# Optimization experiments

Hardware: AMD Instinct MI355X
Metric: run time of the kernel (lower is better)

The kernel has to match this reference:

```python
import jax, jax.numpy as jnp
import numpy as np

N_SAMPLES = 8_000_000
N_TRAIN = 1_000_000
KS = 9
HALF_KS = (KS - 1) // 2  # 4
SIGMA = 1.0


def _build_stats():
    """Replicates LDSLoss.__init__: histogramdd, gaussian LDS smoothing, scaling."""
    rng = np.random.default_rng(0)
    labels = rng.uniform(0.0, 10.0, size=(N_TRAIN, 2))
    n_bins = int((labels.max() - labels.min()) / 0.1)
    hist, edges = np.histogramdd(labels, bins=n_bins)
    # gaussian_filter1d(impulse, sigma)/max == exp(-0.5*(x/sigma)^2), truncated at 4*sigma (= half_ks)
    x = np.arange(-HALF_KS, HALF_KS + 1, dtype=np.float64)
    kernel = np.exp(-0.5 * (x / SIGMA) ** 2)
    # scipy.ndimage.convolve1d(hist, kernel, mode='constant') acts along the LAST axis only;
    # kernel is symmetric so convolution == correlation.
    pad = np.pad(hist, ((0, 0), (HALF_KS, HALF_KS)))
    smoothed = np.zeros_like(hist)
    for k in range(KS):
        smoothed += kernel[k] * pad[:, k:k + n_bins]
    bins0 = edges[0]
    bins1 = edges[1]
    # scaling = len(w)/sum(w) with w = 1/smoothed[bin(label)] over the training labels
    i0 = np.clip(np.searchsorted(bins0, labels[:, 0], side='right') - 1, 0, n_bins - 1)
    i1 = np.clip(np.searchsorted(bins1, labels[:, 1], side='right') - 1, 0, n_bins - 1)
    w = 1.0 / smoothed[i0, i1]
    scaling = len(w) / w.sum()
    lo = np.array([bins0[0], bins1[0]])
    hi = np.array([bins0[-1], bins1[-1]])
    return (smoothed.astype(np.float32), bins0.astype(np.float32),
            bins1.astype(np.float32), np.float32(scaling), lo, hi)


def setup_inputs() -> dict:
    smoothed, bins0, bins1, scaling, lo, hi = _build_stats()
    key = jax.random.key(0)
    k1, k2 = jax.random.split(key)
    inp = jax.random.normal(k1, (N_SAMPLES, 2), dtype=jnp.float32)
    # targets drawn inside the training-label range (as histogram bins cover it)
    tgt = jax.random.uniform(k2, (N_SAMPLES, 2), dtype=jnp.float32,
                             minval=jnp.asarray(lo, jnp.float32),
                             maxval=jnp.asarray(hi, jnp.float32))
    return {
        "input": inp,
        "target": tgt,
        "smoothed_distribution": jnp.asarray(smoothed),
        "bins0": jnp.asarray(bins0),
        "bins1": jnp.asarray(bins1),
        "scaling": jnp.asarray(scaling),
    }


def reference(input, target, smoothed_distribution, bins0, bins1, scaling):
    nb = smoothed_distribution.shape[0]
    # torch.where(label < bins)[0][0] - 1  ==  searchsorted(bins, label, 'right') - 1,
    # with the 'no edge greater' case mapped to the last bin (len(bins)-2).
    i0 = jnp.clip(jnp.searchsorted(bins0, target[:, 0], side='right') - 1, 0, nb - 1)
    i1 = jnp.clip(jnp.searchsorted(bins1, target[:, 1], side='right') - 1, 0, nb - 1)
    kernel_weights = smoothed_distribution[i0, i1]          # irregular gather  [N]
    weights = 1.0 / kernel_weights
    inf_mask = jnp.isinf(weights)
    finite_max = jnp.max(jnp.where(inf_mask, -jnp.inf, weights))
    weights = jnp.where(inf_mask, finite_max, weights) * scaling
    loss = (input - target) ** 2                             # MSELoss(reduction='none')
    loss = loss * weights[:, None]
    return jnp.mean(loss)
```

## Files before the change

### kernel.cpp

```cpp
#include <hip/hip_runtime.h>
#include <math.h>


#define BLOCK 1024
#define GRID_BLKS 512

__device__ __forceinline__ int find_bin(const float* __restrict__ sb, int nb,
                                        float x, float lo, float inv_step) {
    int g = (int)floorf((x - lo) * inv_step);
    g = g < 0 ? 0 : (g > nb - 1 ? nb - 1 : g);
    float e0 = sb[g];
    float e1 = sb[g + 1];
    g += (x >= e1) ? 1 : 0;
    g -= (x < e0) ? 1 : 0;
    return g < 0 ? 0 : (g > nb - 1 ? nb - 1 : g);
}

__device__ __forceinline__ void process_pair(
    float4 in, float4 tg,
    float* __restrict__ hist,
    const float* __restrict__ sb0, const float* __restrict__ sb1, int nb,
    float lo0, float inv0, float lo1, float inv1)
{
    float dA0 = in.x - tg.x, dA1 = in.y - tg.y;
    float sqA = dA0 * dA0 + dA1 * dA1;
    int iA0 = find_bin(sb0, nb, tg.x, lo0, inv0);
    int iA1 = find_bin(sb1, nb, tg.y, lo1, inv1);
    atomicAdd(&hist[iA0 * nb + iA1], sqA);

    float dB0 = in.z - tg.z, dB1 = in.w - tg.w;
    float sqB = dB0 * dB0 + dB1 * dB1;
    int iB0 = find_bin(sb0, nb, tg.z, lo0, inv0);
    int iB1 = find_bin(sb1, nb, tg.w, lo1, inv1);
    atomicAdd(&hist[iB0 * nb + iB1], sqB);
}

__global__ void __launch_bounds__(BLOCK, 8)
lds_loss_hist(const float* __restrict__ input,
              const float* __restrict__ target,
              const float* __restrict__ smoothed,
              const float* __restrict__ bins0,
              const float* __restrict__ bins1,
              const float* __restrict__ scaling,
              int nb, long long n, long long nelem,
              double* __restrict__ accA,
              double* __restrict__ accB,
              unsigned int* __restrict__ accM,
              unsigned int* __restrict__ done_ctr,
              float* __restrict__ out)
{
    extern __shared__ __align__(16) float smem[];
    float* hist = smem;
    float* sb0  = smem + nb * nb;
    float* sb1  = sb0 + (nb + 1);

    const int nbnb = nb * nb;
    for (int i = threadIdx.x; i < nbnb; i += BLOCK) hist[i] = 0.0f;
    for (int i = threadIdx.x; i < nb + 1; i += BLOCK) {
        sb0[i] = bins0[i];
        sb1[i] = bins1[i];
    }
    __syncthreads();

    const float lo0 = sb0[0], inv0 = (float)nb / (sb0[nb] - sb0[0]);
    const float lo1 = sb1[0], inv1 = (float)nb / (sb1[nb] - sb1[0]);

    const long long npair = n >> 1;
    const float4* in4 = (const float4*)input;
    const float4* tg4 = (const float4*)target;
    const long long S = (long long)gridDim.x * BLOCK;
    const long long STEP = 2 * S;

    long long base = (long long)blockIdx.x * BLOCK + threadIdx.x;

    float4 ai0, ai1, at0, at1;
    float4 bi0, bi1, bt0, bt1;

    bool haveA = (base + S) < npair;
    if (haveA) {
        ai0 = in4[base]; ai1 = in4[base + S];
        at0 = tg4[base]; at1 = tg4[base + S];
    }
    while (haveA) {
        long long nxtB = base + STEP;
        bool haveB = (nxtB + S) < npair;
        if (haveB) {
            bi0 = in4[nxtB]; bi1 = in4[nxtB + S];
            bt0 = tg4[nxtB]; bt1 = tg4[nxtB + S];
        }
        __builtin_amdgcn_sched_barrier(0);
        process_pair(ai0, at0, hist, sb0, sb1, nb, lo0, inv0, lo1, inv1);
        process_pair(ai1, at1, hist, sb0, sb1, nb, lo0, inv0, lo1, inv1);
        if (!haveB) { base = nxtB; haveA = false; break; }

        long long nxtA = nxtB + STEP;
        haveA = (nxtA + S) < npair;
        if (haveA) {
            ai0 = in4[nxtA]; ai1 = in4[nxtA + S];
            at0 = tg4[nxtA]; at1 = tg4[nxtA + S];
        }
        __builtin_amdgcn_sched_barrier(0);
        process_pair(bi0, bt0, hist, sb0, sb1, nb, lo0, inv0, lo1, inv1);
        process_pair(bi1, bt1, hist, sb0, sb1, nb, lo0, inv0, lo1, inv1);
        base = nxtA;
    }
    for (long long r = base; r < npair; r += S) {
        process_pair(in4[r], tg4[r], hist, sb0, sb1, nb, lo0, inv0, lo1, inv1);
    }

    if ((n & 1) && blockIdx.x == 0 && threadIdx.x == 0) {
        long long i = n - 1;
        float t0 = target[2 * i], t1 = target[2 * i + 1];
        float d0 = input[2 * i] - t0, d1 = input[2 * i + 1] - t1;
        float sq = d0 * d0 + d1 * d1;
        int j0 = find_bin(sb0, nb, t0, lo0, inv0);
        int j1 = find_bin(sb1, nb, t1, lo1, inv1);
        atomicAdd(&hist[j0 * nb + j1], sq);
    }
    __syncthreads();

    double A = 0.0, B = 0.0;
    float  m = 0.0f;
    for (int b = threadIdx.x; b < nbnb; b += BLOCK) {
        float h = hist[b];
        float s = smoothed[b];
        float w = 1.0f / s;
        if (isinf(w)) {
            B += (double)h;
        } else {
            A += (double)w * (double)h;
            if (h > 0.0f) m = fmaxf(m, w);
        }
    }

    #pragma unroll
    for (int off = 32; off > 0; off >>= 1) {
        A += __shfl_down(A, off, 64);
        B += __shfl_down(B, off, 64);
        m = fmaxf(m, __shfl_down(m, off, 64));
    }

    __shared__ double rA[BLOCK / 64], rB[BLOCK / 64];
    __shared__ float  rM[BLOCK / 64];
    int wave = threadIdx.x >> 6;
    int lane = threadIdx.x & 63;
    if (lane == 0) { rA[wave] = A; rB[wave] = B; rM[wave] = m; }
    __syncthreads();

    if (threadIdx.x == 0) {
        double ta = 0.0, tb = 0.0; float tm = 0.0f;
        #pragma unroll
        for (int w2 = 0; w2 < BLOCK / 64; ++w2) {
            ta += rA[w2]; tb += rB[w2]; tm = fmaxf(tm, rM[w2]);
        }
        atomicAdd(accA, ta);
        atomicAdd(accB, tb);
        atomicMax(accM, __float_as_uint(tm));
        __threadfence();
        unsigned int prev = atomicAdd(done_ctr, 1u);
        if (prev == gridDim.x - 1) {
            double Af = atomicAdd(accA, 0.0);
            double Bf = atomicAdd(accB, 0.0);
            float  Mf = __uint_as_float(atomicMax(accM, 0u));
            double v = (double)(*scaling) * (Af + (double)Mf * Bf) / (double)nelem;
            *out = (float)v;
        }
    }
}

extern "C" void kernel_launch(void* const* d_in, const int* in_sizes, int n_in,
                              void* d_out, int out_size, void* d_ws, size_t ws_size,
                              hipStream_t stream) {
    const float* input    = (const float*)d_in[0];
    const float* target   = (const float*)d_in[1];
    const float* smoothed = (const float*)d_in[2];
    const float* bins0    = (const float*)d_in[3];
    const float* bins1    = (const float*)d_in[4];
    const float* scaling  = (const float*)d_in[5];

    const long long nelem = in_sizes[0];
    const long long n     = nelem / 2;
    const int nb          = in_sizes[3] - 1;

    double*       accA = (double*)d_ws;
    double*       accB = accA + 1;
    unsigned int* accM = (unsigned int*)(accB + 1);
    unsigned int* ctr  = accM + 1;

    hipMemsetAsync(d_ws, 0, 24, stream);

    long long blocks_needed = (n / 2 + BLOCK - 1) / BLOCK;
    int grid = (int)(blocks_needed < GRID_BLKS ? blocks_needed : GRID_BLKS);
    if (grid < 1) grid = 1;
    size_t shmem = ((size_t)nb * nb + 2 * (nb + 1)) * sizeof(float);

    lds_loss_hist<<<grid, BLOCK, shmem, stream>>>(
        input, target, smoothed, bins0, bins1, scaling,
        nb, n, nelem, accA, accB, accM, ctr, (float*)d_out);
}
```

Measured before the change: 188.7 us.

## Pack bin edges as float2, halve block size, use 4-way unrolled load loop

Stores bin edge pairs as float2 in LDS so each bin lookup does one 8-byte LDS read instead of two scalar reads. Replaces the double-buffered A/B prefetch loop with a simpler loop that issues four float4 loads per stream before processing. Changes block size to 512 with grid 1024, giving more blocks and more per-block LDS histograms (each histogram is about 40KB, so LDS limits blocks per CU). The cost is more per-block histogram init and final reduction work, and less cross-iteration prefetch overlap.

```diff
diff --git a/kernel.cpp b/kernel.cpp
--- a/kernel.cpp
+++ b/kernel.cpp
@@ -2,40 +2,39 @@
 #include <math.h>
 
 
-#define BLOCK 1024
-#define GRID_BLKS 512
+#define BLOCK 512
+#define GRID_BLKS 1024
 
-__device__ __forceinline__ int find_bin(const float* __restrict__ sb, int nb,
+__device__ __forceinline__ int find_bin(const float2* __restrict__ ep, int nb,
                                         float x, float lo, float inv_step) {
     int g = (int)floorf((x - lo) * inv_step);
     g = g < 0 ? 0 : (g > nb - 1 ? nb - 1 : g);
-    float e0 = sb[g];
-    float e1 = sb[g + 1];
-    g += (x >= e1) ? 1 : 0;
-    g -= (x < e0) ? 1 : 0;
+    float2 e = ep[g];
+    g += (x >= e.y) ? 1 : 0;
+    g -= (x < e.x) ? 1 : 0;
     return g < 0 ? 0 : (g > nb - 1 ? nb - 1 : g);
 }
 
 __device__ __forceinline__ void process_pair(
     float4 in, float4 tg,
     float* __restrict__ hist,
-    const float* __restrict__ sb0, const float* __restrict__ sb1, int nb,
+    const float2* __restrict__ ep0, const float2* __restrict__ ep1, int nb,
     float lo0, float inv0, float lo1, float inv1)
 {
     float dA0 = in.x - tg.x, dA1 = in.y - tg.y;
     float sqA = dA0 * dA0 + dA1 * dA1;
-    int iA0 = find_bin(sb0, nb, tg.x, lo0, inv0);
-    int iA1 = find_bin(sb1, nb, tg.y, lo1, inv1);
+    int iA0 = find_bin(ep0, nb, tg.x, lo0, inv0);
+    int iA1 = find_bin(ep1, nb, tg.y, lo1, inv1);
     atomicAdd(&hist[iA0 * nb + iA1], sqA);
 
     float dB0 = in.z - tg.z, dB1 = in.w - tg.w;
     float sqB = dB0 * dB0 + dB1 * dB1;
-    int iB0 = find_bin(sb0, nb, tg.z, lo0, inv0);
-    int iB1 = find_bin(sb1, nb, tg.w, lo1, inv1);
+    int iB0 = find_bin(ep0, nb, tg.z, lo0, inv0);
+    int iB1 = find_bin(ep1, nb, tg.w, lo1, inv1);
     atomicAdd(&hist[iB0 * nb + iB1], sqB);
 }
 
-__global__ void __launch_bounds__(BLOCK, 8)
+__global__ void __launch_bounds__(BLOCK, 4)
 lds_loss_hist(const float* __restrict__ input,
               const float* __restrict__ target,
               const float* __restrict__ smoothed,
@@ -50,62 +49,47 @@
               float* __restrict__ out)
 {
     extern __shared__ __align__(16) float smem[];
-    float* hist = smem;
-    float* sb0  = smem + nb * nb;
-    float* sb1  = sb0 + (nb + 1);
+    float2* ep0  = (float2*)smem;
+    float2* ep1  = ep0 + nb;
+    float*  hist = (float*)(ep1 + nb);
 
     const int nbnb = nb * nb;
     for (int i = threadIdx.x; i < nbnb; i += BLOCK) hist[i] = 0.0f;
-    for (int i = threadIdx.x; i < nb + 1; i += BLOCK) {
-        sb0[i] = bins0[i];
-        sb1[i] = bins1[i];
+    for (int i = threadIdx.x; i < nb; i += BLOCK) {
+        ep0[i] = make_float2(bins0[i], bins0[i + 1]);
+        ep1[i] = make_float2(bins1[i], bins1[i + 1]);
     }
     __syncthreads();
 
-    const float lo0 = sb0[0], inv0 = (float)nb / (sb0[nb] - sb0[0]);
-    const float lo1 = sb1[0], inv1 = (float)nb / (sb1[nb] - sb1[0]);
+    const float lo0 = ep0[0].x, hi0 = ep0[nb - 1].y;
+    const float lo1 = ep1[0].x, hi1 = ep1[nb - 1].y;
+    const float inv0 = (float)nb / (hi0 - lo0);
+    const float inv1 = (float)nb / (hi1 - lo1);
 
     const long long npair = n >> 1;
     const float4* in4 = (const float4*)input;
     const float4* tg4 = (const float4*)target;
     const long long S = (long long)gridDim.x * BLOCK;
-    const long long STEP = 2 * S;
 
-    long long base = (long long)blockIdx.x * BLOCK + threadIdx.x;
+    long long p = (long long)blockIdx.x * BLOCK + threadIdx.x;
 
-    float4 ai0, ai1, at0, at1;
-    float4 bi0, bi1, bt0, bt1;
-
-    bool haveA = (base + S) < npair;
-    if (haveA) {
-        ai0 = in4[base]; ai1 = in4[base + S];
-        at0 = tg4[base]; at1 = tg4[base + S];
+    for (; p + 3 * S < npair; p += 4 * S) {
+        float4 I0 = in4[p];
+        float4 I1 = in4[p + S];
+        float4 I2 = in4[p + 2 * S];
+        float4 I3 = in4[p + 3 * S];
+        float4 T0 = tg4[p];
+        float4 T1 = tg4[p + S];
+        float4 T2 = tg4[p + 2 * S];
+        float4 T3 = tg4[p + 3 * S];
+        __builtin_amdgcn_sched_barrier(0);
+        process_pair(I0, T0, hist, ep0, ep1, nb, lo0, inv0, lo1, inv1);
+        process_pair(I1, T1, hist, ep0, ep1, nb, lo0, inv0, lo1, inv1);
+        process_pair(I2, T2, hist, ep0, ep1, nb, lo0, inv0, lo1, inv1);
+        process_pair(I3, T3, hist, ep0, ep1, nb, lo0, inv0, lo1, inv1);
     }
-    while (haveA) {
-        long long nxtB = base + STEP;
-        bool haveB = (nxtB + S) < npair;
-        if (haveB) {
-            bi0 = in4[nxtB]; bi1 = in4[nxtB + S];
-            bt0 = tg4[nxtB]; bt1 = tg4[nxtB + S];
-        }
-        __builtin_amdgcn_sched_barrier(0);
-        process_pair(ai0, at0, hist, sb0, sb1, nb, lo0, inv0, lo1, inv1);
-        process_pair(ai1, at1, hist, sb0, sb1, nb, lo0, inv0, lo1, inv1);
-        if (!haveB) { base = nxtB; haveA = false; break; }
-
-        long long nxtA = nxtB + STEP;
-        haveA = (nxtA + S) < npair;
-        if (haveA) {
-            ai0 = in4[nxtA]; ai1 = in4[nxtA + S];
-            at0 = tg4[nxtA]; at1 = tg4[nxtA + S];
-        }
-        __builtin_amdgcn_sched_barrier(0);
-        process_pair(bi0, bt0, hist, sb0, sb1, nb, lo0, inv0, lo1, inv1);
-        process_pair(bi1, bt1, hist, sb0, sb1, nb, lo0, inv0, lo1, inv1);
-        base = nxtA;
-    }
-    for (long long r = base; r < npair; r += S) {
-        process_pair(in4[r], tg4[r], hist, sb0, sb1, nb, lo0, inv0, lo1, inv1);
+    for (; p < npair; p += S) {
+        process_pair(in4[p], tg4[p], hist, ep0, ep1, nb, lo0, inv0, lo1, inv1);
     }
 
     if ((n & 1) && blockIdx.x == 0 && threadIdx.x == 0) {
@@ -113,8 +97,8 @@
         float t0 = target[2 * i], t1 = target[2 * i + 1];
         float d0 = input[2 * i] - t0, d1 = input[2 * i + 1] - t1;
         float sq = d0 * d0 + d1 * d1;
-        int j0 = find_bin(sb0, nb, t0, lo0, inv0);
-        int j1 = find_bin(sb1, nb, t1, lo1, inv1);
+        int j0 = find_bin(ep0, nb, t0, lo0, inv0);
+        int j1 = find_bin(ep1, nb, t1, lo1, inv1);
         atomicAdd(&hist[j0 * nb + j1], sq);
     }
     __syncthreads();
@@ -192,7 +176,7 @@
     long long blocks_needed = (n / 2 + BLOCK - 1) / BLOCK;
     int grid = (int)(blocks_needed < GRID_BLKS ? blocks_needed : GRID_BLKS);
     if (grid < 1) grid = 1;
-    size_t shmem = ((size_t)nb * nb + 2 * (nb + 1)) * sizeof(float);
+    size_t shmem = ((size_t)nb * nb + 4 * (size_t)nb) * sizeof(float);
 
     lds_loss_hist<<<grid, BLOCK, shmem, stream>>>(
         input, target, smoothed, bins0, bins1, scaling,
```

After: 207.3 us. 1.1x slower.
